# Kernel optimization log

Measured on AMD Instinct MI355X. Metric: run time of the kernel, lower is better.

## Reference

```python
import jax, jax.numpy as jnp
import numpy as np

B, S, D = 2, 2048, 2048
H, HKV = 32, 8
HD = D // H  # 64
NEG_INF = -1e9


def _rope_tables(seq_len, head_dim):
    inv_freq = 1.0 / (10000.0 ** (np.arange(0, head_dim, 2, dtype=np.float32) / head_dim))
    t = np.arange(seq_len, dtype=np.float32)
    freqs = np.outer(t, inv_freq)                      # (S, HD/2)
    emb = np.concatenate([freqs, freqs], axis=-1)      # (S, HD)
    cos = np.cos(emb)[None, None]                      # (1,1,S,HD)
    sin = np.sin(emb)[None, None]
    return jnp.asarray(cos), jnp.asarray(sin)


def setup_inputs() -> dict:
    key = jax.random.key(0)
    ks = jax.random.split(key, 5)
    hidden_states = jax.random.normal(ks[0], (B, S, D), dtype=jnp.float32)
    # causal additive mask: 0 where allowed, -inf (large negative) where masked
    causal = jnp.tril(jnp.ones((S, S), dtype=jnp.bool_))
    attention_mask = jnp.where(causal, 0.0, NEG_INF).astype(jnp.float32)
    attention_mask = jnp.broadcast_to(attention_mask[None, None], (B, 1, S, S))
    cos, sin = _rope_tables(S, HD)
    sc = 0.02
    Wq = jax.random.normal(ks[1], (D, H * HD), dtype=jnp.float32) * sc
    Wk = jax.random.normal(ks[2], (D, HKV * HD), dtype=jnp.float32) * sc
    Wv = jax.random.normal(ks[3], (D, HKV * HD), dtype=jnp.float32) * sc
    Wo = jax.random.normal(ks[4], (H * HD, D), dtype=jnp.float32) * sc
    return {"hidden_states": hidden_states, "attention_mask": attention_mask,
            "cos": cos, "sin": sin, "Wq": Wq, "Wk": Wk, "Wv": Wv, "Wo": Wo}


def _rotate_half(x):
    x1, x2 = jnp.split(x, 2, axis=-1)
    return jnp.concatenate([-x2, x1], axis=-1)


def _apply_rope(x, cos, sin):
    # x: (B, h, S, HD); cos/sin: (1,1,S,HD)
    return x * cos + _rotate_half(x) * sin


def reference(hidden_states, attention_mask, cos, sin, Wq, Wk, Wv, Wo):
    b, s, _ = hidden_states.shape
    scale = 1.0 / np.sqrt(HD)
    q = (hidden_states @ Wq).reshape(b, s, H, HD).transpose(0, 2, 1, 3)    # (B,H,S,HD)
    k = (hidden_states @ Wk).reshape(b, s, HKV, HD).transpose(0, 2, 1, 3)  # (B,HKV,S,HD)
    v = (hidden_states @ Wv).reshape(b, s, HKV, HD).transpose(0, 2, 1, 3)
    q = _apply_rope(q, cos, sin)
    k = _apply_rope(k, cos, sin)
    # GQA: group query heads per kv head without materializing repeated KV
    g = H // HKV
    qg = q.reshape(b, HKV, g, s, HD)
    scores = jnp.einsum('bkgqd,bksd->bkgqs', qg, k) * scale               # (B,HKV,g,S,S)
    scores = scores + attention_mask[:, :, None]                          # broadcast (B,1,1,S,S)
    attn = jax.nn.softmax(scores, axis=-1)
    out = jnp.einsum('bkgqs,bksd->bkgqd', attn, v)                        # (B,HKV,g,S,HD)
    out = out.reshape(b, H, s, HD).transpose(0, 2, 1, 3).reshape(b, s, H * HD)
    return out @ Wo
```

## Files before the change

kernel.cpp:

```cpp
#include <hip/hip_runtime.h>
#include <math.h>

typedef _Float16 half8 __attribute__((ext_vector_type(8)));
typedef _Float16 half4 __attribute__((ext_vector_type(4)));
typedef _Float16 half2 __attribute__((ext_vector_type(2)));
typedef float f32x4 __attribute__((ext_vector_type(4)));

#define S_LEN 2048
#define DM    2048
#define NH    32
#define NKV   8

#define QSCALE 0.1803368801111204f
#define NSHIFT -11.541560327111707f

#if __has_builtin(__builtin_amdgcn_exp2f)
#define EXP2(x) __builtin_amdgcn_exp2f(x)
#else
#define EXP2(x) __builtin_exp2f(x)
#endif

__device__ __forceinline__ half2 pkrtz(float a, float b) {
    return __builtin_bit_cast(half2, __builtin_amdgcn_cvt_pkrtz(a, b));
}

__device__ __forceinline__ void async16(const void* g, void* l) {
    __builtin_amdgcn_global_load_lds(
        (const __attribute__((address_space(1))) unsigned int*)g,
        (__attribute__((address_space(3))) unsigned int*)l, 16, 0, 0);
}

__global__ __launch_bounds__(256) void cast_h(const float* __restrict__ x,
                                              _Float16* __restrict__ y, int n)
{
    int i = (blockIdx.x * 256 + threadIdx.x) * 4;
    if (i >= n) return;
    float4 v = *(const float4*)(x + i);
    half4 o = {(_Float16)v.x, (_Float16)v.y, (_Float16)v.z, (_Float16)v.w};
    *(half4*)(y + i) = o;
}

__global__ __launch_bounds__(256) void transpose_all(
    const float* __restrict__ Wq, const float* __restrict__ Wk,
    const float* __restrict__ Wv, const float* __restrict__ Wo,
    _Float16* __restrict__ Wqkv_t, _Float16* __restrict__ Wo_t)
{
    const int z = blockIdx.z;
    const float* W; _Float16* Wt; int N;
    if (z == 0)      { W = Wq; Wt = Wqkv_t;                        N = 2048; }
    else if (z == 1) { W = Wk; Wt = Wqkv_t + (size_t)2048 * 2048;  N = 512;  }
    else if (z == 2) { W = Wv; Wt = Wqkv_t + (size_t)2560 * 2048;  N = 512;  }
    else             { W = Wo; Wt = Wo_t;                          N = 2048; }
    if ((int)blockIdx.x * 32 >= N) return;

    __shared__ float t[32][33];
    const int n0 = blockIdx.x * 32, k0 = blockIdx.y * 32;
    const int tx = threadIdx.x & 31, ty = threadIdx.x >> 5;
#pragma unroll
    for (int i = 0; i < 32; i += 8)
        t[ty + i][tx] = W[(size_t)(k0 + ty + i) * N + n0 + tx];
    __syncthreads();
#pragma unroll
    for (int i = 0; i < 32; i += 8)
        Wt[(size_t)(n0 + ty + i) * 2048 + k0 + tx] = (_Float16)t[tx][ty + i];
}

__global__ __launch_bounds__(512, 2) void gemm_h(
    const _Float16* __restrict__ A, const _Float16* __restrict__ Bt,
    void* __restrict__ Cout, int N, int K, int mode,
    const float* __restrict__ cosT, const float* __restrict__ sinT)
{
    __shared__ __align__(16) _Float16 Lds[2][4][8192];
    const int tid  = threadIdx.x;
    const int lane = tid & 63;
    const int wave = tid >> 6;
    const int lm = lane & 15, quad = lane >> 4;
    const int wm = wave >> 2;
    const int wn = wave & 3;

    const int gx  = gridDim.x;
    const int nwg = gx * gridDim.y;
    const int lin = blockIdx.y * gx + blockIdx.x;
    const int tsw = (lin & 7) * (nwg >> 3) + (lin >> 3);
    const int bm  = (tsw / gx) * 256, bn = (tsw % gx) * 256;
    const int nt  = K >> 6;

    const int sr   = tid >> 3;
    const int lg   = (tid & 7) ^ (sr & 7);
    const int grow = sr * 2 + (lg >> 2);
    const int gcol = (lg & 3) << 3;
    const _Float16* pA0 = A  + (size_t)(bm + grow) * K + gcol;
    const _Float16* pB0 = Bt + (size_t)(bn + grow) * K + gcol;
    char* ldsb = (char*)Lds + tid * 16;

#define STAGE(t, idx) do { if ((t) < nt) {                          \
        const int koff_ = (t) * 64 + (((idx) >> 1) << 5);           \
        const _Float16* s_ = (((idx) & 1) ? pA0 : pB0) + koff_;     \
        char* d_ = ldsb + (((t) & 1) << 16) + ((idx) << 14);        \
        async16(s_, d_);                                            \
        async16(s_ + (size_t)128 * K, d_ + 8192);                   \
    } } while (0)

    const int chsw = (((((lm & 1) << 2) | quad) ^ (lm >> 1)) << 3);
    const int ar = (wm << 6) + (lm >> 1);
    const int br = (wn << 5) + (lm >> 1);
    const _Float16* Lh = (const _Float16*)Lds;

    f32x4 acc[8][4];
#pragma unroll
    for (int i = 0; i < 8; ++i)
#pragma unroll
        for (int j = 0; j < 4; ++j) acc[i][j] = (f32x4){0.f, 0.f, 0.f, 0.f};

    STAGE(0, 0); STAGE(0, 1); STAGE(0, 2); STAGE(0, 3);
    STAGE(1, 0); STAGE(1, 1); STAGE(1, 2);
    if (nt > 1) asm volatile("s_waitcnt vmcnt(6)" ::: "memory");
    else        asm volatile("s_waitcnt vmcnt(0)" ::: "memory");
    __builtin_amdgcn_s_barrier();

    half8 af[4], bf[4];
#define MFMA16(mb)                                                            \
    _Pragma("unroll") for (int i_ = 0; i_ < 4; ++i_)                          \
    _Pragma("unroll") for (int j_ = 0; j_ < 4; ++j_)                          \
        acc[(mb) + i_][j_] = __builtin_amdgcn_mfma_f32_16x16x32_f16(          \
            af[i_], bf[j_], acc[(mb) + i_][j_], 0, 0, 0);

#define PH_BAR()  __builtin_amdgcn_s_barrier();                               \
                  asm volatile("s_waitcnt lgkmcnt(0)" ::: "memory");          \
                  __builtin_amdgcn_s_setprio(1)
#define PH_END()  __builtin_amdgcn_s_setprio(0);                              \
                  __builtin_amdgcn_s_barrier()

    int p = 0;
    for (int G = 0; G < nt; ++G, p ^= 1) {
        const _Float16* Lp = Lh + (p << 15);
        const _Float16* Au0 = Lp + 8192  + ar * 64 + chsw;
        const _Float16* Au1 = Lp + 24576 + ar * 64 + chsw;
        const _Float16* Bu0 = Lp +         br * 64 + chsw;
        const _Float16* Bu1 = Lp + 16384 + br * 64 + chsw;
#pragma unroll
        for (int i = 0; i < 4; ++i) af[i] = *(const half8*)(Au0 + i * 512);
#pragma unroll
        for (int j = 0; j < 4; ++j) bf[j] = *(const half8*)(Bu0 + j * 512);
        STAGE(G + 1, 3);
        PH_BAR(); MFMA16(0); PH_END();
#pragma unroll
        for (int i = 0; i < 4; ++i) af[i] = *(const half8*)(Au0 + 2048 + i * 512);
        STAGE(G + 2, 0);
        PH_BAR(); MFMA16(4); PH_END();
#pragma unroll
        for (int i = 0; i < 4; ++i) af[i] = *(const half8*)(Au1 + i * 512);
#pragma unroll
        for (int j = 0; j < 4; ++j) bf[j] = *(const half8*)(Bu1 + j * 512);
        STAGE(G + 2, 1);
        PH_BAR(); MFMA16(0); PH_END();
#pragma unroll
        for (int i = 0; i < 4; ++i) af[i] = *(const half8*)(Au1 + 2048 + i * 512);
        STAGE(G + 2, 2);
        PH_BAR(); MFMA16(4);
        __builtin_amdgcn_s_setprio(0);
        if (G + 2 < nt) asm volatile("s_waitcnt vmcnt(6)" ::: "memory");
        else            asm volatile("s_waitcnt vmcnt(0)" ::: "memory");
        __builtin_amdgcn_s_barrier();
    }
#undef STAGE
#undef MFMA16
#undef PH_BAR
#undef PH_END

    const int mrowq = bm + (wm << 7) + (quad << 2);
    if (mode == 0) {
        float* C = (float*)Cout;
        const int col0 = bn + (wn << 6) + lm;
#pragma unroll
        for (int mf = 0; mf < 8; ++mf)
#pragma unroll
            for (int r = 0; r < 4; ++r) {
                const int m = mrowq + mf * 16 + r;
#pragma unroll
                for (int nf = 0; nf < 4; ++nf)
                    C[(size_t)m * N + col0 + nf * 16] = acc[mf][nf][r];
            }
        return;
    }

    _Float16* Cq = (_Float16*)Cout;
    _Float16* Ck = Cq + (size_t)2 * NH * S_LEN * 64;
    _Float16* Cv = Ck + (size_t)2 * NKV * S_LEN * 64;
    const int colbase = bn + (wn << 6);
    const int region = (colbase >= 2560) ? 2 : (colbase >= 2048) ? 1 : 0;

    if (region == 2) {
        const int head = (colbase - 2560) >> 6;
#pragma unroll
        for (int mf = 0; mf < 8; ++mf) {
            const int m0 = mrowq + mf * 16;
            const int b = m0 >> 11, s0 = m0 & 2047;
#pragma unroll
            for (int nf = 0; nf < 4; ++nf) {
                half2 lo = pkrtz(acc[mf][nf][0], acc[mf][nf][1]);
                half2 hi = pkrtz(acc[mf][nf][2], acc[mf][nf][3]);
                half4 ov = {lo[0], lo[1], hi[0], hi[1]};
                *(half4*)(Cv + ((((size_t)b * NKV + head) << 6) + lm + nf * 16) * S_LEN + s0) = ov;
            }
        }
        return;
    }

    const float qscale = (region == 0) ? QSCALE : 1.0f;
    const int head = (region == 0) ? (colbase >> 6) : ((colbase - 2048) >> 6);
    _Float16* Cdst = (region == 0) ? Cq : Ck;
    const int nh = (region == 0) ? NH : NKV;
#pragma unroll
    for (int mf = 0; mf < 8; ++mf)
#pragma unroll
        for (int r = 0; r < 4; ++r) {
            int m = mrowq + mf * 16 + r;
            int b = m >> 11, s = m & 2047;
            const float* cp = cosT + s * 64 + lm;
            const float* sp = sinT + s * 64 + lm;
            float a0r = acc[mf][0][r], a1r = acc[mf][1][r];
            float a2r = acc[mf][2][r], a3r = acc[mf][3][r];
            float o0 = (a0r * cp[0]  - a2r * sp[0])  * qscale;
            float o1 = (a1r * cp[16] - a3r * sp[16]) * qscale;
            float o2 = (a2r * cp[32] + a0r * sp[32]) * qscale;
            float o3 = (a3r * cp[48] + a1r * sp[48]) * qscale;
            _Float16* d = Cdst + ((((size_t)b * nh + head) * S_LEN + s) << 6) + lm;
            d[0]  = (_Float16)o0;
            d[16] = (_Float16)o1;
            d[32] = (_Float16)o2;
            d[48] = (_Float16)o3;
        }
}

#define LSWOFS(row, halfofs) \
    ((row) * 64 + (((((halfofs) >> 3) & 7) ^ ((row) & 7)) << 3) + ((halfofs) & 7))

__global__ __launch_bounds__(256, 2) void attn_h(
    const _Float16* __restrict__ q, const _Float16* __restrict__ k,
    const _Float16* __restrict__ vt, _Float16* __restrict__ x2)
{
    __shared__ __align__(16) _Float16 Ks[64 * 64];
    __shared__ __align__(16) _Float16 Vts[64 * 64];

    const int kvh = blockIdx.y, b = blockIdx.z;
    const int tid = threadIdx.x;
    const int wave = tid >> 6, lane = tid & 63;
    const int lm = lane & 15, quad = lane >> 4;
    const int h = kvh * 4 + wave;

    const int qtT[2] = {63 - (int)blockIdx.x, (int)blockIdx.x};
    const int ktm[2] = {(qtT[0] * 32 + 31) >> 6, (qtT[1] * 32 + 31) >> 6};

    const _Float16* kbase  = k  + ((((size_t)b * NKV + kvh) * S_LEN) << 6);
    const _Float16* vtbase = vt + ((((size_t)b * NKV + kvh) << 6) * S_LEN);

    half8 qf[2][2][2];
#pragma unroll
    for (int tp = 0; tp < 2; ++tp) {
        const _Float16* qb = q + ((((size_t)b * NH + h) * S_LEN + qtT[tp] * 32) << 6);
#pragma unroll
        for (int i = 0; i < 2; ++i)
#pragma unroll
            for (int kk = 0; kk < 2; ++kk)
                qf[tp][i][kk] = *(const half8*)(qb + (i * 16 + lm) * 64 + kk * 32 + quad * 8);
    }

    f32x4 accOT[2][2][4];
    float lpart[2][2];
#pragma unroll
    for (int tp = 0; tp < 2; ++tp)
#pragma unroll
        for (int i = 0; i < 2; ++i) {
            lpart[tp][i] = 0.f;
#pragma unroll
            for (int j = 0; j < 4; ++j) accOT[tp][i][j] = (f32x4){0.f, 0.f, 0.f, 0.f};
        }

    const int f0 = tid * 16, f1 = 4096 + tid * 16;
    const int r0 = f0 >> 7, r1 = f1 >> 7;
    const int c0 = ((f0 >> 4) & 7) ^ (r0 & 7);
    const int c1 = ((f1 >> 4) & 7) ^ (r1 & 7);

    for (int kt = 0; kt <= ktm[0]; ++kt) {
        async16((const char*)kbase + (size_t)kt * 8192 + r0 * 128 + c0 * 16, (char*)Ks + f0);
        async16((const char*)kbase + (size_t)kt * 8192 + r1 * 128 + c1 * 16, (char*)Ks + f1);
        async16((const char*)vtbase + (size_t)r0 * 4096 + kt * 128 + c0 * 16, (char*)Vts + f0);
        async16((const char*)vtbase + (size_t)r1 * 4096 + kt * 128 + c1 * 16, (char*)Vts + f1);
        __syncthreads();

        half8 kf[4][2];
        half4 vtf[4][4];
#pragma unroll
        for (int t = 0; t < 4; ++t) {
#pragma unroll
            for (int kk = 0; kk < 2; ++kk)
                kf[t][kk] = *(const half8*)(Ks + LSWOFS(t * 16 + lm, kk * 32 + quad * 8));
#pragma unroll
            for (int j = 0; j < 4; ++j)
                vtf[j][t] = *(const half4*)(Vts + LSWOFS(j * 16 + lm, t * 16 + quad * 4));
        }

#pragma unroll
        for (int tp = 0; tp < 2; ++tp) {
            if (kt > ktm[tp]) continue;
            const bool diag = (kt == ktm[tp]);
#pragma unroll
            for (int i = 0; i < 2; ++i) {
                f32x4 sc[4];
#pragma unroll
                for (int t = 0; t < 4; ++t) {
                    f32x4 z = (f32x4){NSHIFT, NSHIFT, NSHIFT, NSHIFT};
                    z = __builtin_amdgcn_mfma_f32_16x16x32_f16(kf[t][0], qf[tp][i][0], z, 0, 0, 0);
                    z = __builtin_amdgcn_mfma_f32_16x16x32_f16(kf[t][1], qf[tp][i][1], z, 0, 0, 0);
                    sc[t] = z;
                }
                if (diag) {
                    const int qpos = qtT[tp] * 32 + i * 16 + lm;
#pragma unroll
                    for (int t = 0; t < 4; ++t)
#pragma unroll
                        for (int r = 0; r < 4; ++r) {
                            int key = kt * 64 + t * 16 + quad * 4 + r;
                            if (key > qpos) sc[t][r] = -30000.f;
                        }
                }
                half4 pt[4];
                float lp = 0.f;
#pragma unroll
                for (int t = 0; t < 4; ++t) {
                    float p0 = EXP2(sc[t][0]), p1 = EXP2(sc[t][1]);
                    float p2 = EXP2(sc[t][2]), p3 = EXP2(sc[t][3]);
                    lp += (p0 + p1) + (p2 + p3);
                    half2 lo = pkrtz(p0, p1);
                    half2 hi = pkrtz(p2, p3);
                    pt[t] = (half4){lo[0], lo[1], hi[0], hi[1]};
                }
                lpart[tp][i] += lp;
#pragma unroll
                for (int j = 0; j < 4; ++j)
#pragma unroll
                    for (int t = 0; t < 4; ++t)
                        accOT[tp][i][j] = __builtin_amdgcn_mfma_f32_16x16x16f16(
                            vtf[j][t], pt[t], accOT[tp][i][j], 0, 0, 0);
            }
        }
        __syncthreads();
    }

#pragma unroll
    for (int tp = 0; tp < 2; ++tp)
#pragma unroll
        for (int i = 0; i < 2; ++i) {
            float l = lpart[tp][i];
            l += __shfl_xor(l, 16);
            l += __shfl_xor(l, 32);
            const float inv = 1.f / l;
            const size_t row = (size_t)b * S_LEN + qtT[tp] * 32 + i * 16 + lm;
#pragma unroll
            for (int j = 0; j < 4; ++j) {
                f32x4 o = accOT[tp][i][j];
                half2 lo = pkrtz(o[0] * inv, o[1] * inv);
                half2 hi = pkrtz(o[2] * inv, o[3] * inv);
                half4 ov = {lo[0], lo[1], hi[0], hi[1]};
                *(half4*)(x2 + row * DM + h * 64 + j * 16 + quad * 4) = ov;
            }
        }
}

extern "C" void kernel_launch(void* const* d_in, const int* in_sizes, int n_in,
                              void* d_out, int out_size, void* d_ws, size_t ws_size,
                              hipStream_t stream)
{
    const float* hidden = (const float*)d_in[0];
    const float* cosT = (const float*)d_in[2];
    const float* sinT = (const float*)d_in[3];
    const float* Wq = (const float*)d_in[4];
    const float* Wk = (const float*)d_in[5];
    const float* Wv = (const float*)d_in[6];
    const float* Wo = (const float*)d_in[7];
    float* out = (float*)d_out;

    _Float16* w = (_Float16*)d_ws;
    _Float16* hid_h  = w;  w += (size_t)4096 * 2048;
    _Float16* Wqkv_t = w;  w += (size_t)3072 * 2048;
    _Float16* Wo_t   = w;  w += (size_t)2048 * 2048;
    _Float16* qh     = w;  w += (size_t)2 * NH * S_LEN * 64;
    _Float16* kh     = w;  w += (size_t)2 * NKV * S_LEN * 64;
    _Float16* vth    = w;  w += (size_t)2 * NKV * S_LEN * 64;
    _Float16* x2h    = w;

    dim3 blk(256);
    cast_h<<<dim3(8192), blk, 0, stream>>>(hidden, hid_h, 8388608);
    transpose_all<<<dim3(64, 64, 4), blk, 0, stream>>>(Wq, Wk, Wv, Wo, Wqkv_t, Wo_t);

    gemm_h<<<dim3(12, 16), dim3(512), 0, stream>>>(hid_h, Wqkv_t, qh, 3072, 2048, 1, cosT, sinT);

    attn_h<<<dim3(32, 8, 2), blk, 0, stream>>>(qh, kh, vth, x2h);

    gemm_h<<<dim3(8, 16), dim3(512), 0, stream>>>(x2h, Wo_t, out, 2048, 2048, 0, nullptr, nullptr);
}
```

Measured before the change: 321.1 us.

## Double-buffer K/V tiles in attention and add MFMA priority hints

The attention kernel now keeps two LDS buffers for K and V^T and issues the async loads for the next key tile before computing on the current one, so global-load latency overlaps with MFMA work instead of stalling on a barrier each iteration. MFMA sections are wrapped in s_setprio to favour matrix issue across waves. Separately, the RoPE epilogue reuses the cos/sin values at offsets 0 and 16 in place of also loading offsets 32 and 48, relying on the duplicated table layout. LDS use doubles, which may affect occupancy at two blocks per CU.

```diff
diff --git a/kernel.cpp b/kernel.cpp
--- a/kernel.cpp
+++ b/kernel.cpp
@@ -217,14 +217,14 @@
         for (int r = 0; r < 4; ++r) {
             int m = mrowq + mf * 16 + r;
             int b = m >> 11, s = m & 2047;
-            const float* cp = cosT + s * 64 + lm;
-            const float* sp = sinT + s * 64 + lm;
+            const float c0 = cosT[s * 64 + lm], c16 = cosT[s * 64 + lm + 16];
+            const float s0 = sinT[s * 64 + lm], s16 = sinT[s * 64 + lm + 16];
             float a0r = acc[mf][0][r], a1r = acc[mf][1][r];
             float a2r = acc[mf][2][r], a3r = acc[mf][3][r];
-            float o0 = (a0r * cp[0]  - a2r * sp[0])  * qscale;
-            float o1 = (a1r * cp[16] - a3r * sp[16]) * qscale;
-            float o2 = (a2r * cp[32] + a0r * sp[32]) * qscale;
-            float o3 = (a3r * cp[48] + a1r * sp[48]) * qscale;
+            float o0 = (a0r * c0  - a2r * s0)  * qscale;
+            float o1 = (a1r * c16 - a3r * s16) * qscale;
+            float o2 = (a2r * c0  + a0r * s0)  * qscale;
+            float o3 = (a3r * c16 + a1r * s16) * qscale;
             _Float16* d = Cdst + ((((size_t)b * nh + head) * S_LEN + s) << 6) + lm;
             d[0]  = (_Float16)o0;
             d[16] = (_Float16)o1;
@@ -240,8 +240,8 @@
     const _Float16* __restrict__ q, const _Float16* __restrict__ k,
     const _Float16* __restrict__ vt, _Float16* __restrict__ x2)
 {
-    __shared__ __align__(16) _Float16 Ks[64 * 64];
-    __shared__ __align__(16) _Float16 Vts[64 * 64];
+    __shared__ __align__(16) _Float16 Ks[2][64 * 64];
+    __shared__ __align__(16) _Float16 Vts[2][64 * 64];
 
     const int kvh = blockIdx.y, b = blockIdx.z;
     const int tid = threadIdx.x;
@@ -281,13 +281,27 @@
     const int r0 = f0 >> 7, r1 = f1 >> 7;
     const int c0 = ((f0 >> 4) & 7) ^ (r0 & 7);
     const int c1 = ((f1 >> 4) & 7) ^ (r1 & 7);
+    const char* ksrc0 = (const char*)kbase  + r0 * 128 + c0 * 16;
+    const char* ksrc1 = (const char*)kbase  + r1 * 128 + c1 * 16;
+    const char* vsrc0 = (const char*)vtbase + (size_t)r0 * 4096 + c0 * 16;
+    const char* vsrc1 = (const char*)vtbase + (size_t)r1 * 4096 + c1 * 16;
+
+#define STAGEKV(kt, nb) do {                                          \
+        async16(ksrc0 + (size_t)(kt) * 8192, (char*)Ks[nb]  + f0);    \
+        async16(ksrc1 + (size_t)(kt) * 8192, (char*)Ks[nb]  + f1);    \
+        async16(vsrc0 + (kt) * 128,          (char*)Vts[nb] + f0);    \
+        async16(vsrc1 + (kt) * 128,          (char*)Vts[nb] + f1);    \
+    } while (0)
+
+    STAGEKV(0, 0);
+    asm volatile("s_waitcnt vmcnt(0)" ::: "memory");
+    __builtin_amdgcn_s_barrier();
 
     for (int kt = 0; kt <= ktm[0]; ++kt) {
-        async16((const char*)kbase + (size_t)kt * 8192 + r0 * 128 + c0 * 16, (char*)Ks + f0);
-        async16((const char*)kbase + (size_t)kt * 8192 + r1 * 128 + c1 * 16, (char*)Ks + f1);
-        async16((const char*)vtbase + (size_t)r0 * 4096 + kt * 128 + c0 * 16, (char*)Vts + f0);
-        async16((const char*)vtbase + (size_t)r1 * 4096 + kt * 128 + c1 * 16, (char*)Vts + f1);
-        __syncthreads();
+        const int cur = kt & 1;
+        if (kt < ktm[0]) STAGEKV(kt + 1, cur ^ 1);
+        const _Float16* Kc = Ks[cur];
+        const _Float16* Vc = Vts[cur];
 
         half8 kf[4][2];
         half4 vtf[4][4];
@@ -295,10 +309,10 @@
         for (int t = 0; t < 4; ++t) {
 #pragma unroll
             for (int kk = 0; kk < 2; ++kk)
-                kf[t][kk] = *(const half8*)(Ks + LSWOFS(t * 16 + lm, kk * 32 + quad * 8));
+                kf[t][kk] = *(const half8*)(Kc + LSWOFS(t * 16 + lm, kk * 32 + quad * 8));
 #pragma unroll
             for (int j = 0; j < 4; ++j)
-                vtf[j][t] = *(const half4*)(Vts + LSWOFS(j * 16 + lm, t * 16 + quad * 4));
+                vtf[j][t] = *(const half4*)(Vc + LSWOFS(j * 16 + lm, t * 16 + quad * 4));
         }
 
 #pragma unroll
@@ -308,6 +322,7 @@
 #pragma unroll
             for (int i = 0; i < 2; ++i) {
                 f32x4 sc[4];
+                __builtin_amdgcn_s_setprio(1);
 #pragma unroll
                 for (int t = 0; t < 4; ++t) {
                     f32x4 z = (f32x4){NSHIFT, NSHIFT, NSHIFT, NSHIFT};
@@ -315,6 +330,7 @@
                     z = __builtin_amdgcn_mfma_f32_16x16x32_f16(kf[t][1], qf[tp][i][1], z, 0, 0, 0);
                     sc[t] = z;
                 }
+                __builtin_amdgcn_s_setprio(0);
                 if (diag) {
                     const int qpos = qtT[tp] * 32 + i * 16 + lm;
 #pragma unroll
@@ -337,16 +353,20 @@
                     pt[t] = (half4){lo[0], lo[1], hi[0], hi[1]};
                 }
                 lpart[tp][i] += lp;
+                __builtin_amdgcn_s_setprio(1);
 #pragma unroll
                 for (int j = 0; j < 4; ++j)
 #pragma unroll
                     for (int t = 0; t < 4; ++t)
                         accOT[tp][i][j] = __builtin_amdgcn_mfma_f32_16x16x16f16(
                             vtf[j][t], pt[t], accOT[tp][i][j], 0, 0, 0);
+                __builtin_amdgcn_s_setprio(0);
             }
         }
-        __syncthreads();
+        asm volatile("s_waitcnt vmcnt(0)" ::: "memory");
+        __builtin_amdgcn_s_barrier();
     }
+#undef STAGEKV
 
 #pragma unroll
     for (int tp = 0; tp < 2; ++tp)
```

After: 323.1 us. About the same (+0.6%).
